# Kernel optimization log

Hardware: AMD Instinct MI355X
Metric: run time of the kernel (lower is better)

## Reference

```python
import jax, jax.numpy as jnp
import numpy as np


def setup_inputs() -> dict:
    key = jax.random.key(0)
    k1, k2, k3 = jax.random.split(key, 3)
    bs, S, d, C = 2, 196, 512, 1006
    imgFeaturemap = jax.random.normal(k1, (bs, S, d), dtype=jnp.float32)
    wordFeatures = jax.random.normal(k2, (C, d), dtype=jnp.float32)
    fc3_w = jax.random.normal(k3, (d, d), dtype=jnp.float32) * 0.02
    fc3_b = jnp.zeros((d,), dtype=jnp.float32)
    return {"imgFeaturemap": imgFeaturemap, "wordFeatures": wordFeatures,
            "fc3_w": fc3_w, "fc3_b": fc3_b}


def reference(imgFeaturemap, wordFeatures, fc3_w, fc3_b):
    # imgFeaturemap: (bs, S, d); wordFeatures: (C, d)
    # Broadcast multiply + tanh: (bs, S, C, d)
    t = jnp.tanh(imgFeaturemap[:, :, None, :] * wordFeatures[None, None, :, :])
    # Per-row Linear (PyTorch Linear: x @ W^T + b)
    feat = jnp.einsum('bscd,ed->bsce', t, fc3_w) + fc3_b
    # Softmax over spatial axis S (axis=1), independently per (class, channel)
    coef = jax.nn.softmax(feat, axis=1)
    # Softmax-weighted spatial pooling per class: (bs, C, d)
    semanticFeature = jnp.einsum('bsd,bscd->bcd', imgFeaturemap, coef)
    return semanticFeature
```

## Files before the change

kernel.cpp:

```cpp
#include <hip/hip_runtime.h>

using half8   = __attribute__((ext_vector_type(8))) _Float16;
using floatx4 = __attribute__((ext_vector_type(4))) float;

namespace {
constexpr int S = 196, D = 512, C = 1006, Cpad = 1024;
constexpr int CB = 16;
constexpr int EBLK = 256;
constexpr int BK = 64;
constexpr int TPB = 256;
constexpr int SCH = 3;
constexpr int RS = 64;
constexpr float KTANH = 2.885390082f;
constexpr float INVK  = 0.34657359028f;

constexpr size_t W16_BYTES = (size_t)D * D * 2;
constexpr size_t LA_OFF    = W16_BYTES;
constexpr size_t SLICE_ELEMS = (size_t)2 * Cpad * D;
constexpr size_t SL_BYTES  = (size_t)SCH * SLICE_ELEMS * 4;
constexpr size_t SLICE_NEED = LA_OFF + 2 * SL_BYTES;
constexpr size_t L_BYTES   = SLICE_ELEMS * 4;

__device__ __forceinline__ int sw_off(int row, int seg) {
    return row * RS + ((seg ^ (row & 7)) << 3);
}

__device__ __forceinline__ void gload16(const _Float16* g, _Float16* l) {
    __builtin_amdgcn_global_load_lds(
        (const __attribute__((address_space(1))) unsigned int*)g,
        (__attribute__((address_space(3))) unsigned int*)l, 16, 0, 0);
}

__device__ __forceinline__ _Float16 tanh_ps(float y) {
    float e = __builtin_amdgcn_exp2f(y);
    return (_Float16)(1.0f - 2.0f * __builtin_amdgcn_rcpf(e + 1.0f));
}

__global__ void prep_w16sw(const float* __restrict__ fw, _Float16* __restrict__ W16sw) {
    int id = blockIdx.x * blockDim.x + threadIdx.x;
    int kki = id >> 12;
    int r   = (id >> 3) & 511;
    int j   = id & 7;
    const float* src = fw + (size_t)r * D + kki * 64 + j * 8;
    floatx4 v0 = *(const floatx4*)src;
    floatx4 v1 = *(const floatx4*)(src + 4);
    half8 h;
    h[0] = (_Float16)v0[0]; h[1] = (_Float16)v0[1];
    h[2] = (_Float16)v0[2]; h[3] = (_Float16)v0[3];
    h[4] = (_Float16)v1[0]; h[5] = (_Float16)v1[1];
    h[6] = (_Float16)v1[2]; h[7] = (_Float16)v1[3];
    *(half8*)&W16sw[((size_t)kki << 15) + r * RS + ((j ^ (r & 7)) << 3)] = h;
}

__global__ __launch_bounds__(TPB, 3) void semdec_mfma(
    const float* __restrict__ img, const float* __restrict__ word,
    const _Float16* __restrict__ W16sw,
    float* __restrict__ lbase, float* __restrict__ abase, int use_slice)
{
    __shared__ __align__(16) _Float16 Wc[EBLK * RS];
    __shared__ __align__(16) _Float16 Tc[4 * CB * RS];
    __shared__ __align__(16) float imgS[4][D];

    const int ct = blockIdx.x;
    const int et = blockIdx.y & 1;
    const int b  = blockIdx.y >> 1;
    const int sc = blockIdx.z;

    const int tid  = threadIdx.x;
    const int lane = tid & 63;
    const int ew   = tid >> 6;
    const int l15  = lane & 15;
    const int quad = lane >> 4;

    const int c0 = ct * CB;
    const int e0 = et * EBLK;

    floatx4 lacc[4], aacc[4];
    #pragma unroll
    for (int ej = 0; ej < 4; ++ej) {
        lacc[ej] = (floatx4){0.f, 0.f, 0.f, 0.f};
        aacc[ej] = (floatx4){0.f, 0.f, 0.f, 0.f};
    }

    const float* imgB = img + (size_t)b * S * D;
    const int s_base = sc * 66;
    const int npass = (sc < 2) ? 17 : 16;

    for (int pr = 0; pr < npass; ++pr) {
        const int s0 = s_base + pr * 4;
        const int slim = (pr == 16) ? 2 : 4;

        __syncthreads();
        #pragma unroll
        for (int it = 0; it < 2; ++it) {
            int sid = it * TPB + tid;
            int si = sid >> 7, pos = (sid & 127) << 2;
            floatx4 v = *(const floatx4*)&imgB[(size_t)(s0 + si) * D + pos];
            floatx4 sv = {v[0] * KTANH, v[1] * KTANH, v[2] * KTANH, v[3] * KTANH};
            *(floatx4*)&imgS[si][pos] = sv;
        }

        floatx4 acc[4][4];
        #pragma unroll
        for (int si = 0; si < 4; ++si)
            #pragma unroll
            for (int ej = 0; ej < 4; ++ej)
                acc[si][ej] = (floatx4){0.f, 0.f, 0.f, 0.f};

        for (int kk = 0; kk < D; kk += BK) {
            const int kki = kk >> 6;
            __syncthreads();
            {
                const _Float16* wg = W16sw + ((size_t)kki << 15) + ((size_t)e0 << 6);
                #pragma unroll
                for (int it = 0; it < 8; ++it) {
                    int o = ((ew * 8 + it) << 9) + (lane << 3);
                    gload16(wg + o, &Wc[o]);
                }
            }
            #pragma unroll
            for (int it = 0; it < 2; ++it) {
                int sid = it * TPB + tid;
                int si = sid >> 7, rem = sid & 127;
                int ci = rem >> 3, seg = rem & 7;
                int cg = c0 + ci; if (cg > C - 1) cg = C - 1;
                const float* wp = &word[(size_t)cg * D + kk + seg * 8];
                floatx4 w0 = *(const floatx4*)wp;
                floatx4 w1 = *(const floatx4*)(wp + 4);
                const float* ip = &imgS[si][kk + seg * 8];
                floatx4 i0 = *(const floatx4*)ip;
                floatx4 i1 = *(const floatx4*)(ip + 4);
                half8 t;
                t[0] = tanh_ps(i0[0] * w0[0]);
                t[1] = tanh_ps(i0[1] * w0[1]);
                t[2] = tanh_ps(i0[2] * w0[2]);
                t[3] = tanh_ps(i0[3] * w0[3]);
                t[4] = tanh_ps(i1[0] * w1[0]);
                t[5] = tanh_ps(i1[1] * w1[1]);
                t[6] = tanh_ps(i1[2] * w1[2]);
                t[7] = tanh_ps(i1[3] * w1[3]);
                *(half8*)&Tc[sw_off(si * CB + ci, seg)] = t;
            }
            __syncthreads();
            #pragma unroll
            for (int k2 = 0; k2 < 2; ++k2) {
                const int jb = (k2 << 2) + quad;
                half8 bf[4], af[4];
                #pragma unroll
                for (int ej = 0; ej < 4; ++ej)
                    bf[ej] = *(const half8*)&Wc[sw_off(ew * 64 + ej * 16 + l15, jb)];
                #pragma unroll
                for (int si = 0; si < 4; ++si)
                    af[si] = *(const half8*)&Tc[sw_off(si * CB + l15, jb)];
                #pragma unroll
                for (int si = 0; si < 4; ++si)
                    #pragma unroll
                    for (int ej = 0; ej < 4; ++ej)
                        acc[si][ej] = __builtin_amdgcn_mfma_f32_16x16x32_f16(
                            af[si], bf[ej], acc[si][ej], 0, 0, 0);
            }
        }
        #pragma unroll
        for (int si = 0; si < 4; ++si) {
            if (si >= slim) break;
            #pragma unroll
            for (int ej = 0; ej < 4; ++ej) {
                float ie = imgS[si][e0 + ew * 64 + ej * 16 + l15] * INVK;
                #pragma unroll
                for (int r = 0; r < 4; ++r) {
                    float ev = __builtin_amdgcn_exp2f(acc[si][ej][r] * 1.44269504f);
                    lacc[ej][r] += ev;
                    aacc[ej][r] += ie * ev;
                }
            }
        }
    }

    if (use_slice) {
        float* lsl = lbase + (size_t)sc * SLICE_ELEMS;
        float* asl = abase + (size_t)sc * SLICE_ELEMS;
        #pragma unroll
        for (int r = 0; r < 4; ++r) {
            int cg = c0 + quad * 4 + r;
            #pragma unroll
            for (int ej = 0; ej < 4; ++ej) {
                int eg = e0 + ew * 64 + ej * 16 + l15;
                size_t o = ((size_t)b * Cpad + cg) * D + eg;
                lsl[o] = lacc[ej][r];
                asl[o] = aacc[ej][r];
            }
        }
    } else {
        #pragma unroll
        for (int r = 0; r < 4; ++r) {
            int cg = c0 + quad * 4 + r;
            #pragma unroll
            for (int ej = 0; ej < 4; ++ej) {
                int eg = e0 + ew * 64 + ej * 16 + l15;
                atomicAdd(&lbase[((size_t)b * Cpad + cg) * D + eg], lacc[ej][r]);
                if (cg < C)
                    atomicAdd(&abase[((size_t)b * C + cg) * D + eg], aacc[ej][r]);
            }
        }
    }
}

__global__ void finalize_k(const float* __restrict__ lbase, const float* __restrict__ abase,
                           float* __restrict__ out, int use_slice) {
    int o = blockIdx.x * blockDim.x + threadIdx.x;
    if (o >= 2 * C * D) return;
    int b = o / (C * D);
    int rem = o - b * (C * D);
    int c = rem >> 9;
    int e = rem & (D - 1);
    size_t p = ((size_t)b * Cpad + c) * D + e;
    if (use_slice) {
        float l = 0.f, a = 0.f;
        #pragma unroll
        for (int scn = 0; scn < SCH; ++scn) {
            l += lbase[(size_t)scn * SLICE_ELEMS + p];
            a += abase[(size_t)scn * SLICE_ELEMS + p];
        }
        out[o] = a / l;
    } else {
        out[o] = out[o] / lbase[p];
    }
}

}

extern "C" void kernel_launch(void* const* d_in, const int* in_sizes, int n_in,
                              void* d_out, int out_size, void* d_ws, size_t ws_size,
                              hipStream_t stream) {
    const float* img  = (const float*)d_in[0];
    const float* word = (const float*)d_in[1];
    const float* fw   = (const float*)d_in[2];
    float* out = (float*)d_out;
    char* ws = (char*)d_ws;

    _Float16* W16sw = (_Float16*)ws;
    const int use_slice = (ws_size >= SLICE_NEED) ? 1 : 0;

    hipLaunchKernelGGL(prep_w16sw, dim3(128), dim3(256), 0, stream, fw, W16sw);

    float *lbase, *abase;
    if (use_slice) {
        lbase = (float*)(ws + LA_OFF);
        abase = (float*)(ws + LA_OFF + SL_BYTES);
    } else {
        lbase = (float*)(ws + LA_OFF);
        abase = out;
        hipMemsetAsync(lbase, 0, L_BYTES, stream);
        hipMemsetAsync(out, 0, (size_t)2 * C * D * 4, stream);
    }

    hipLaunchKernelGGL(semdec_mfma, dim3(64, 4, SCH), dim3(TPB), 0, stream,
                       img, word, W16sw, lbase, abase, use_slice);

    hipLaunchKernelGGL(finalize_k, dim3((2 * C * D + 255) / 256), dim3(256), 0, stream,
                       lbase, abase, out, use_slice);
}
```

Baseline: 374.7 us.

## Double-buffer W and tanh tiles in LDS with BK=32 software pipelining

```diff
diff --git a/kernel.cpp b/kernel.cpp
--- a/kernel.cpp
+++ b/kernel.cpp
@@ -7,10 +7,10 @@
 constexpr int S = 196, D = 512, C = 1006, Cpad = 1024;
 constexpr int CB = 16;
 constexpr int EBLK = 256;
-constexpr int BK = 64;
+constexpr int BK = 32;
+constexpr int NCH = D / BK;
 constexpr int TPB = 256;
 constexpr int SCH = 3;
-constexpr int RS = 64;
 constexpr float KTANH = 2.885390082f;
 constexpr float INVK  = 0.34657359028f;
 
@@ -21,8 +21,10 @@
 constexpr size_t SLICE_NEED = LA_OFF + 2 * SL_BYTES;
 constexpr size_t L_BYTES   = SLICE_ELEMS * 4;
 
-__device__ __forceinline__ int sw_off(int row, int seg) {
-    return row * RS + ((seg ^ (row & 7)) << 3);
+__device__ __forceinline__ int phys16(int row, int j) {
+    int p = row >> 1;
+    int q = ((((row & 1) << 2) | j) ^ (p & 7));
+    return p * 8 + q;
 }
 
 __device__ __forceinline__ void gload16(const _Float16* g, _Float16* l) {
@@ -38,10 +40,10 @@
 
 __global__ void prep_w16sw(const float* __restrict__ fw, _Float16* __restrict__ W16sw) {
     int id = blockIdx.x * blockDim.x + threadIdx.x;
-    int kki = id >> 12;
-    int r   = (id >> 3) & 511;
-    int j   = id & 7;
-    const float* src = fw + (size_t)r * D + kki * 64 + j * 8;
+    int kki = id >> 11;
+    int rem = id & 2047;
+    int r = rem >> 2, j = rem & 3;
+    const float* src = fw + (size_t)r * D + kki * BK + j * 8;
     floatx4 v0 = *(const floatx4*)src;
     floatx4 v1 = *(const floatx4*)(src + 4);
     half8 h;
@@ -49,7 +51,7 @@
     h[2] = (_Float16)v0[2]; h[3] = (_Float16)v0[3];
     h[4] = (_Float16)v1[0]; h[5] = (_Float16)v1[1];
     h[6] = (_Float16)v1[2]; h[7] = (_Float16)v1[3];
-    *(half8*)&W16sw[((size_t)kki << 15) + r * RS + ((j ^ (r & 7)) << 3)] = h;
+    *(half8*)&W16sw[((size_t)kki << 14) + (phys16(r, j) << 3)] = h;
 }
 
 __global__ __launch_bounds__(TPB, 3) void semdec_mfma(
@@ -57,8 +59,8 @@
     const _Float16* __restrict__ W16sw,
     float* __restrict__ lbase, float* __restrict__ abase, int use_slice)
 {
-    __shared__ __align__(16) _Float16 Wc[EBLK * RS];
-    __shared__ __align__(16) _Float16 Tc[4 * CB * RS];
+    __shared__ __align__(16) _Float16 Wc[2][EBLK * BK];
+    __shared__ __align__(16) _Float16 Tc[2][4 * CB * BK];
     __shared__ __align__(16) float imgS[4][D];
 
     const int ct = blockIdx.x;
@@ -68,12 +70,17 @@
 
     const int tid  = threadIdx.x;
     const int lane = tid & 63;
-    const int ew   = tid >> 6;
+    const int wv   = tid >> 6;
     const int l15  = lane & 15;
     const int quad = lane >> 4;
+    const int ciT  = lane & 15;
+    const int jgT  = lane >> 4;
 
     const int c0 = ct * CB;
     const int e0 = et * EBLK;
+
+    int cgT = c0 + ciT; if (cgT > C - 1) cgT = C - 1;
+    const float* wordRow = word + (size_t)cgT * D;
 
     floatx4 lacc[4], aacc[4];
     #pragma unroll
@@ -99,6 +106,7 @@
             floatx4 sv = {v[0] * KTANH, v[1] * KTANH, v[2] * KTANH, v[3] * KTANH};
             *(floatx4*)&imgS[si][pos] = sv;
         }
+        __syncthreads();
 
         floatx4 acc[4][4];
         #pragma unroll
@@ -107,65 +115,78 @@
             for (int ej = 0; ej < 4; ++ej)
                 acc[si][ej] = (floatx4){0.f, 0.f, 0.f, 0.f};
 
-        for (int kk = 0; kk < D; kk += BK) {
-            const int kki = kk >> 6;
+        {
+            const _Float16* wg = W16sw + ((size_t)e0 << 5);
+            #pragma unroll
+            for (int it = 0; it < 4; ++it) {
+                int o = (wv * 4 + it) * 512 + (lane << 3);
+                gload16(wg + o, &Wc[0][o]);
+            }
+            const float* wp = wordRow + jgT * 8;
+            floatx4 w0 = *(const floatx4*)wp;
+            floatx4 w1 = *(const floatx4*)(wp + 4);
+            const float* ip = &imgS[wv][jgT * 8];
+            floatx4 i0 = *(const floatx4*)ip;
+            floatx4 i1 = *(const floatx4*)(ip + 4);
+            half8 t;
+            t[0] = tanh_ps(i0[0] * w0[0]); t[1] = tanh_ps(i0[1] * w0[1]);
+            t[2] = tanh_ps(i0[2] * w0[2]); t[3] = tanh_ps(i0[3] * w0[3]);
+            t[4] = tanh_ps(i1[0] * w1[0]); t[5] = tanh_ps(i1[1] * w1[1]);
+            t[6] = tanh_ps(i1[2] * w1[2]); t[7] = tanh_ps(i1[3] * w1[3]);
+            *(half8*)&Tc[0][phys16(wv * CB + ciT, jgT) << 3] = t;
+        }
+
+        for (int kki = 0; kki < NCH; ++kki) {
+            const int mb = kki & 1;
             __syncthreads();
-            {
-                const _Float16* wg = W16sw + ((size_t)kki << 15) + ((size_t)e0 << 6);
+
+            floatx4 w0, w1, i0, i1;
+            if (kki < NCH - 1) {
+                const _Float16* wg = W16sw + (((size_t)(kki + 1)) << 14) + ((size_t)e0 << 5);
                 #pragma unroll
-                for (int it = 0; it < 8; ++it) {
-                    int o = ((ew * 8 + it) << 9) + (lane << 3);
-                    gload16(wg + o, &Wc[o]);
+                for (int it = 0; it < 4; ++it) {
+                    int o = (wv * 4 + it) * 512 + (lane << 3);
+                    gload16(wg + o, &Wc[mb ^ 1][o]);
                 }
-            }
-            #pragma unroll
-            for (int it = 0; it < 2; ++it) {
-                int sid = it * TPB + tid;
-                int si = sid >> 7, rem = sid & 127;
-                int ci = rem >> 3, seg = rem & 7;
-                int cg = c0 + ci; if (cg > C - 1) cg = C - 1;
-                const float* wp = &word[(size_t)cg * D + kk + seg * 8];
-                floatx4 w0 = *(const floatx4*)wp;
-                floatx4 w1 = *(const floatx4*)(wp + 4);
-                const float* ip = &imgS[si][kk + seg * 8];
-                floatx4 i0 = *(const floatx4*)ip;
-                floatx4 i1 = *(const floatx4*)(ip + 4);
-                half8 t;
-                t[0] = tanh_ps(i0[0] * w0[0]);
-                t[1] = tanh_ps(i0[1] * w0[1]);
-                t[2] = tanh_ps(i0[2] * w0[2]);
-                t[3] = tanh_ps(i0[3] * w0[3]);
-                t[4] = tanh_ps(i1[0] * w1[0]);
-                t[5] = tanh_ps(i1[1] * w1[1]);
-                t[6] = tanh_ps(i1[2] * w1[2]);
-                t[7] = tanh_ps(i1[3] * w1[3]);
-                *(half8*)&Tc[sw_off(si * CB + ci, seg)] = t;
-            }
-            __syncthreads();
-            #pragma unroll
-            for (int k2 = 0; k2 < 2; ++k2) {
-                const int jb = (k2 << 2) + quad;
-                half8 bf[4], af[4];
+                const int kn = (kki + 1) * BK;
+                const float* wp = wordRow + kn + jgT * 8;
+                w0 = *(const floatx4*)wp;
+                w1 = *(const floatx4*)(wp + 4);
+                const float* ip = &imgS[wv][kn + jgT * 8];
+                i0 = *(const floatx4*)ip;
+                i1 = *(const floatx4*)(ip + 4);
+            }
+
+            half8 bf[4], af[4];
+            #pragma unroll
+            for (int ej = 0; ej < 4; ++ej)
+                bf[ej] = *(const half8*)&Wc[mb][phys16(wv * 64 + ej * 16 + l15, quad) << 3];
+            #pragma unroll
+            for (int si = 0; si < 4; ++si)
+                af[si] = *(const half8*)&Tc[mb][phys16(si * CB + l15, quad) << 3];
+            #pragma unroll
+            for (int si = 0; si < 4; ++si)
                 #pragma unroll
                 for (int ej = 0; ej < 4; ++ej)
-                    bf[ej] = *(const half8*)&Wc[sw_off(ew * 64 + ej * 16 + l15, jb)];
-                #pragma unroll
-                for (int si = 0; si < 4; ++si)
-                    af[si] = *(const half8*)&Tc[sw_off(si * CB + l15, jb)];
-                #pragma unroll
-                for (int si = 0; si < 4; ++si)
-                    #pragma unroll
-                    for (int ej = 0; ej < 4; ++ej)
-                        acc[si][ej] = __builtin_amdgcn_mfma_f32_16x16x32_f16(
-                            af[si], bf[ej], acc[si][ej], 0, 0, 0);
-            }
-        }
+                    acc[si][ej] = __builtin_amdgcn_mfma_f32_16x16x32_f16(
+                        af[si], bf[ej], acc[si][ej], 0, 0, 0);
+
+            if (kki < NCH - 1) {
+                half8 t;
+                t[0] = tanh_ps(i0[0] * w0[0]); t[1] = tanh_ps(i0[1] * w0[1]);
+                t[2] = tanh_ps(i0[2] * w0[2]); t[3] = tanh_ps(i0[3] * w0[3]);
+                t[4] = tanh_ps(i1[0] * w1[0]); t[5] = tanh_ps(i1[1] * w1[1]);
+                t[6] = tanh_ps(i1[2] * w1[2]); t[7] = tanh_ps(i1[3] * w1[3]);
+                *(half8*)&Tc[mb ^ 1][phys16(wv * CB + ciT, jgT) << 3] = t;
+            }
+        }
+
         #pragma unroll
         for (int si = 0; si < 4; ++si) {
             if (si >= slim) break;
             #pragma unroll
             for (int ej = 0; ej < 4; ++ej) {
-                float ie = imgS[si][e0 + ew * 64 + ej * 16 + l15] * INVK;
+                float ie = imgS[si][e0 + wv * 64 + ej * 16 + l15] * INVK;
                 #pragma unroll
                 for (int r = 0; r < 4; ++r) {
                     float ev = __builtin_amdgcn_exp2f(acc[si][ej][r] * 1.44269504f);
@@ -184,7 +205,7 @@
             int cg = c0 + quad * 4 + r;
             #pragma unroll
             for (int ej = 0; ej < 4; ++ej) {
-                int eg = e0 + ew * 64 + ej * 16 + l15;
+                int eg = e0 + wv * 64 + ej * 16 + l15;
                 size_t o = ((size_t)b * Cpad + cg) * D + eg;
                 lsl[o] = lacc[ej][r];
                 asl[o] = aacc[ej][r];
@@ -196,7 +217,7 @@
             int cg = c0 + quad * 4 + r;
             #pragma unroll
             for (int ej = 0; ej < 4; ++ej) {
-                int eg = e0 + ew * 64 + ej * 16 + l15;
+                int eg = e0 + wv * 64 + ej * 16 + l15;
                 atomicAdd(&lbase[((size_t)b * Cpad + cg) * D + eg], lacc[ej][r]);
                 if (cg < C)
                     atomicAdd(&abase[((size_t)b * C + cg) * D + eg], aacc[ej][r]);
```

Result: slower. 415.6 us (+10.9%).

## Split spatial axis into four chunks, raise occupancy, and restructure tanh tile mapping

Applied to the files above, without the earlier changes.

```diff
diff --git a/kernel.cpp b/kernel.cpp
--- a/kernel.cpp
+++ b/kernel.cpp
@@ -9,7 +9,7 @@
 constexpr int EBLK = 256;
 constexpr int BK = 64;
 constexpr int TPB = 256;
-constexpr int SCH = 3;
+constexpr int SCH = 4;
 constexpr int RS = 64;
 constexpr float KTANH = 2.885390082f;
 constexpr float INVK  = 0.34657359028f;
@@ -41,7 +41,7 @@
     int kki = id >> 12;
     int r   = (id >> 3) & 511;
     int j   = id & 7;
-    const float* src = fw + (size_t)r * D + kki * 64 + j * 8;
+    const float* src = fw + (size_t)r * D + kki * BK + j * 8;
     floatx4 v0 = *(const floatx4*)src;
     floatx4 v1 = *(const floatx4*)(src + 4);
     half8 h;
@@ -52,7 +52,7 @@
     *(half8*)&W16sw[((size_t)kki << 15) + r * RS + ((j ^ (r & 7)) << 3)] = h;
 }
 
-__global__ __launch_bounds__(TPB, 3) void semdec_mfma(
+__global__ __launch_bounds__(TPB, 4) void semdec_mfma(
     const float* __restrict__ img, const float* __restrict__ word,
     const _Float16* __restrict__ W16sw,
     float* __restrict__ lbase, float* __restrict__ abase, int use_slice)
@@ -68,12 +68,15 @@
 
     const int tid  = threadIdx.x;
     const int lane = tid & 63;
-    const int ew   = tid >> 6;
+    const int wv   = tid >> 6;
     const int l15  = lane & 15;
     const int quad = lane >> 4;
 
     const int c0 = ct * CB;
     const int e0 = et * EBLK;
+
+    int cgT = c0 + l15; if (cgT > C - 1) cgT = C - 1;
+    const float* wordRow = word + (size_t)cgT * D;
 
     floatx4 lacc[4], aacc[4];
     #pragma unroll
@@ -83,19 +86,19 @@
     }
 
     const float* imgB = img + (size_t)b * S * D;
-    const int s_base = sc * 66;
-    const int npass = (sc < 2) ? 17 : 16;
-
-    for (int pr = 0; pr < npass; ++pr) {
+    const int s_base = sc * 49;
+
+    for (int pr = 0; pr < 13; ++pr) {
         const int s0 = s_base + pr * 4;
-        const int slim = (pr == 16) ? 2 : 4;
+        const int slim = (pr == 12) ? 1 : 4;
 
         __syncthreads();
         #pragma unroll
         for (int it = 0; it < 2; ++it) {
             int sid = it * TPB + tid;
             int si = sid >> 7, pos = (sid & 127) << 2;
-            floatx4 v = *(const floatx4*)&imgB[(size_t)(s0 + si) * D + pos];
+            int srow = s0 + si; if (srow > S - 1) srow = S - 1;
+            floatx4 v = *(const floatx4*)&imgB[(size_t)srow * D + pos];
             floatx4 sv = {v[0] * KTANH, v[1] * KTANH, v[2] * KTANH, v[3] * KTANH};
             *(floatx4*)&imgS[si][pos] = sv;
         }
@@ -114,50 +117,47 @@
                 const _Float16* wg = W16sw + ((size_t)kki << 15) + ((size_t)e0 << 6);
                 #pragma unroll
                 for (int it = 0; it < 8; ++it) {
-                    int o = ((ew * 8 + it) << 9) + (lane << 3);
+                    int o = ((wv * 8 + it) << 9) + (lane << 3);
                     gload16(wg + o, &Wc[o]);
                 }
             }
             #pragma unroll
             for (int it = 0; it < 2; ++it) {
-                int sid = it * TPB + tid;
-                int si = sid >> 7, rem = sid & 127;
-                int ci = rem >> 3, seg = rem & 7;
-                int cg = c0 + ci; if (cg > C - 1) cg = C - 1;
-                const float* wp = &word[(size_t)cg * D + kk + seg * 8];
+                int seg = quad + it * 4;
+                const float* wp = wordRow + kk + seg * 8;
                 floatx4 w0 = *(const floatx4*)wp;
                 floatx4 w1 = *(const floatx4*)(wp + 4);
-                const float* ip = &imgS[si][kk + seg * 8];
+                const float* ip = &imgS[wv][kk + seg * 8];
                 floatx4 i0 = *(const floatx4*)ip;
                 floatx4 i1 = *(const floatx4*)(ip + 4);
                 half8 t;
-                t[0] = tanh_ps(i0[0] * w0[0]);
-                t[1] = tanh_ps(i0[1] * w0[1]);
-                t[2] = tanh_ps(i0[2] * w0[2]);
-                t[3] = tanh_ps(i0[3] * w0[3]);
-                t[4] = tanh_ps(i1[0] * w1[0]);
-                t[5] = tanh_ps(i1[1] * w1[1]);
-                t[6] = tanh_ps(i1[2] * w1[2]);
-                t[7] = tanh_ps(i1[3] * w1[3]);
-                *(half8*)&Tc[sw_off(si * CB + ci, seg)] = t;
+                t[0] = tanh_ps(i0[0] * w0[0]); t[1] = tanh_ps(i0[1] * w0[1]);
+                t[2] = tanh_ps(i0[2] * w0[2]); t[3] = tanh_ps(i0[3] * w0[3]);
+                t[4] = tanh_ps(i1[0] * w1[0]); t[5] = tanh_ps(i1[1] * w1[1]);
+                t[6] = tanh_ps(i1[2] * w1[2]); t[7] = tanh_ps(i1[3] * w1[3]);
+                *(half8*)&Tc[sw_off(wv * CB + l15, seg)] = t;
             }
             __syncthreads();
             #pragma unroll
             for (int k2 = 0; k2 < 2; ++k2) {
                 const int jb = (k2 << 2) + quad;
-                half8 bf[4], af[4];
-                #pragma unroll
-                for (int ej = 0; ej < 4; ++ej)
-                    bf[ej] = *(const half8*)&Wc[sw_off(ew * 64 + ej * 16 + l15, jb)];
+                half8 af[4];
                 #pragma unroll
                 for (int si = 0; si < 4; ++si)
                     af[si] = *(const half8*)&Tc[sw_off(si * CB + l15, jb)];
                 #pragma unroll
-                for (int si = 0; si < 4; ++si)
+                for (int h = 0; h < 2; ++h) {
+                    half8 bf[2];
                     #pragma unroll
-                    for (int ej = 0; ej < 4; ++ej)
-                        acc[si][ej] = __builtin_amdgcn_mfma_f32_16x16x32_f16(
-                            af[si], bf[ej], acc[si][ej], 0, 0, 0);
+                    for (int e2 = 0; e2 < 2; ++e2)
+                        bf[e2] = *(const half8*)&Wc[sw_off(wv * 64 + (h * 2 + e2) * 16 + l15, jb)];
+                    #pragma unroll
+                    for (int si = 0; si < 4; ++si)
+                        #pragma unroll
+                        for (int e2 = 0; e2 < 2; ++e2)
+                            acc[si][h * 2 + e2] = __builtin_amdgcn_mfma_f32_16x16x32_f16(
+                                af[si], bf[e2], acc[si][h * 2 + e2], 0, 0, 0);
+                }
             }
         }
         #pragma unroll
@@ -165,7 +165,7 @@
             if (si >= slim) break;
             #pragma unroll
             for (int ej = 0; ej < 4; ++ej) {
-                float ie = imgS[si][e0 + ew * 64 + ej * 16 + l15] * INVK;
+                float ie = imgS[si][e0 + wv * 64 + ej * 16 + l15] * INVK;
                 #pragma unroll
                 for (int r = 0; r < 4; ++r) {
                     float ev = __builtin_amdgcn_exp2f(acc[si][ej][r] * 1.44269504f);
@@ -184,7 +184,7 @@
             int cg = c0 + quad * 4 + r;
             #pragma unroll
             for (int ej = 0; ej < 4; ++ej) {
-                int eg = e0 + ew * 64 + ej * 16 + l15;
+                int eg = e0 + wv * 64 + ej * 16 + l15;
                 size_t o = ((size_t)b * Cpad + cg) * D + eg;
                 lsl[o] = lacc[ej][r];
                 asl[o] = aacc[ej][r];
@@ -196,7 +196,7 @@
             int cg = c0 + quad * 4 + r;
             #pragma unroll
             for (int ej = 0; ej < 4; ++ej) {
-                int eg = e0 + ew * 64 + ej * 16 + l15;
+                int eg = e0 + wv * 64 + ej * 16 + l15;
                 atomicAdd(&lbase[((size_t)b * Cpad + cg) * D + eg], lacc[ej][r]);
                 if (cg < C)
                     atomicAdd(&abase[((size_t)b * C + cg) * D + eg], aacc[ej][r]);
```

Result: slower. 464.3 us (+23.9%).
